# Performance work log

Measured on AMD Instinct MI355X. Metric: run time of the kernel, lower is better.

The kernel has to match this reference:

```python
import jax, jax.numpy as jnp
import numpy as np

NUM_ITER = 3
HEADS = 8
EPS = 1e-8

def _ln(x, g, b, eps=1e-5):
    mu = x.mean(-1, keepdims=True)
    var = ((x - mu) ** 2).mean(-1, keepdims=True)
    return (x - mu) * jax.lax.rsqrt(var + eps) * g + b

def setup_inputs() -> dict:
    key = jax.random.key(0)
    ks = jax.random.split(key, 10)
    B, Nkv, Din = 32, 4096, 256
    Nq, S, Hm = 16, 256, 512
    def xav(k, shape):
        lim = (6.0 / (shape[0] + shape[1])) ** 0.5
        return jax.random.uniform(k, shape, minval=-lim, maxval=lim, dtype=jnp.float32)
    return {
        "slots": jax.random.normal(ks[0], (Nq, S), dtype=jnp.float32),
        "inputs": jax.random.normal(ks[1], (B, Nkv, Din), dtype=jnp.float32),
        "norm_in_g": jnp.ones((Din,), jnp.float32), "norm_in_b": jnp.zeros((Din,), jnp.float32),
        "norm_slots_g": jnp.ones((S,), jnp.float32), "norm_slots_b": jnp.zeros((S,), jnp.float32),
        "norm_mlp_g": jnp.ones((S,), jnp.float32), "norm_mlp_b": jnp.zeros((S,), jnp.float32),
        "Wq": xav(ks[2], (S, S)), "Wk": xav(ks[3], (S, Din)), "Wv": xav(ks[4], (S, Din)),
        "gru_wih": xav(ks[5], (3 * S, S)),
        "gru_whh": jax.random.normal(ks[6], (3 * S, S), dtype=jnp.float32) * (1.0 / S ** 0.5),
        "gru_bih": jnp.zeros((3 * S,), jnp.float32), "gru_bhh": jnp.zeros((3 * S,), jnp.float32),
        "mlp_w1": xav(ks[7], (Hm, S)), "mlp_b1": jnp.zeros((Hm,), jnp.float32),
        "mlp_w2": xav(ks[8], (S, Hm)), "mlp_b2": jnp.zeros((S,), jnp.float32),
    }

def reference(slots, inputs, norm_in_g, norm_in_b, norm_slots_g, norm_slots_b,
              norm_mlp_g, norm_mlp_b, Wq, Wk, Wv, gru_wih, gru_whh, gru_bih, gru_bhh,
              mlp_w1, mlp_b1, mlp_w2, mlp_b2):
    B, Nkv, Din = inputs.shape
    Nq, S = slots.shape
    H = HEADS
    hd = S // H
    slots = jnp.broadcast_to(slots, (B, Nq, S))
    x = _ln(inputs, norm_in_g, norm_in_b)
    k = (x @ Wk.T).reshape(B, Nkv, H, hd).transpose(0, 2, 1, 3) * (hd ** -0.5)  # [B,H,Nkv,hd]
    v = (x @ Wv.T).reshape(B, Nkv, H, hd).transpose(0, 2, 1, 3)
    attn_vis = None
    for _ in range(NUM_ITER):
        slots_prev = slots
        s = _ln(slots, norm_slots_g, norm_slots_b)
        q = (s @ Wq.T).reshape(B, Nq, H, hd).transpose(0, 2, 1, 3)  # [B,H,Nq,hd]
        # logits [B,Nkv,H*Nq]; softmax jointly over heads and slots per key (slot-axis softmax)
        logits = jnp.einsum('bhkd,bhqd->bkhq', k, q).reshape(B, Nkv, H * Nq)
        attn = jax.nn.softmax(logits, axis=-1).reshape(B, Nkv, H, Nq).transpose(0, 2, 1, 3)  # [B,H,Nkv,Nq]
        attn_vis = attn.sum(1)  # [B,Nkv,Nq]
        attn_n = attn / (attn.sum(axis=2, keepdims=True) + EPS)  # normalize over keys
        updates = jnp.einsum('bhkq,bhkd->bqhd', attn_n, v).reshape(B, Nq, S)
        # GRUCell: gates order r,z,n
        xg = updates.reshape(-1, S)
        h = slots_prev.reshape(-1, S)
        gi = xg @ gru_wih.T + gru_bih
        gh = h @ gru_whh.T + gru_bhh
        ir, iz, inn = jnp.split(gi, 3, axis=-1)
        hr, hz, hn = jnp.split(gh, 3, axis=-1)
        r = jax.nn.sigmoid(ir + hr)
        z = jax.nn.sigmoid(iz + hz)
        n = jnp.tanh(inn + r * hn)
        slots = ((1.0 - z) * n + z * h).reshape(B, Nq, S)
        m = _ln(slots, norm_mlp_g, norm_mlp_b)
        slots = slots + (jax.nn.relu(m @ mlp_w1.T + mlp_b1) @ mlp_w2.T + mlp_b2)
    return (slots, attn_vis)
```

## Files before the change

### kernel.cpp

```cpp
#include <hip/hip_runtime.h>
#include <stdint.h>

typedef unsigned short u16;
typedef __attribute__((ext_vector_type(8))) _Float16 half8;
typedef __attribute__((ext_vector_type(4))) _Float16 half4;
typedef __attribute__((ext_vector_type(4))) float floatx4;

__device__ inline float bflo(unsigned u){ return __uint_as_float(u << 16); }
__device__ inline float bfhi(unsigned u){ return __uint_as_float(u & 0xffff0000u); }
__device__ inline float bf1(u16 v){ return __uint_as_float(((unsigned)v) << 16); }
__device__ inline u16 f2bf(float f){
  unsigned u = __float_as_uint(f);
  u += 0x7fffu + ((u >> 16) & 1u);
  return (u16)(u >> 16);
}
__device__ inline float dot8(uint4 w, float4 a, float4 b, float acc){
  acc = fmaf(bflo(w.x), a.x, acc); acc = fmaf(bfhi(w.x), a.y, acc);
  acc = fmaf(bflo(w.y), a.z, acc); acc = fmaf(bfhi(w.y), a.w, acc);
  acc = fmaf(bflo(w.z), b.x, acc); acc = fmaf(bfhi(w.z), b.y, acc);
  acc = fmaf(bflo(w.w), b.z, acc); acc = fmaf(bfhi(w.w), b.w, acc);
  return acc;
}

#define CW_SLOTS 0
#define CW_GIN   4096
#define CW_BIN   4352
#define CW_GS    4608
#define CW_BS    4864
#define CW_GM    5120
#define CW_BM    5376
#define CW_WQ    5632
#define CW_WK    71168
#define CW_WV    136704
#define CW_WIH   202240
#define CW_WHH   398848
#define CW_BIH   595456
#define CW_BHH   596224
#define CW_W1    596992
#define CW_B1    728064
#define CW_W2    728576
#define CW_B2    859648
#define CW_TOTAL 859904

__global__ void k_flag(const u16* __restrict__ probe, int* __restrict__ flag){
  int t = threadIdx.x;
  int bad = 0;
  #pragma unroll
  for (int i = 0; i < 4; i++){
    float x = bf1(probe[t + i * 256]);
    if (!(fabsf(x) < 1e6f)) bad = 1;
  }
  __shared__ int s;
  if (t == 0) s = 0;
  __syncthreads();
  if (bad) atomicOr(&s, 1);
  __syncthreads();
  if (t == 0) *flag = s;
}

struct CanonArgs { const void* p[18]; };

__global__ void k_canon(CanonArgs a, const int* __restrict__ flag, u16* __restrict__ cw){
  const int off[19] = {CW_SLOTS, CW_GIN, CW_BIN, CW_GS, CW_BS, CW_GM, CW_BM, CW_WQ,
                       CW_WK, CW_WV, CW_WIH, CW_WHH, CW_BIH, CW_BHH, CW_W1, CW_B1,
                       CW_W2, CW_B2, CW_TOTAL};
  int i = blockIdx.x * 256 + threadIdx.x;
  if (i >= CW_TOTAL) return;
  int f32m = *flag;
  int j = 0;
  while (i >= off[j + 1]) j++;
  int local = i - off[j];
  float v = f32m ? ((const float*)a.p[j])[local] : bf1(((const u16*)a.p[j])[local]);
  cw[i] = f2bf(v);
}

__global__ void k_init(const u16* __restrict__ cw, float* __restrict__ slots,
                       _Float16* __restrict__ wkvh)
{
  int idx = blockIdx.x * 256 + threadIdx.x;
  if (idx < 131072){
    float g = bf1(cw[CW_GIN + (idx & 255)]);
    wkvh[idx] = (_Float16)(bf1(cw[CW_WK + idx]) * g);
  } else {
    int i = idx - 131072;
    int d = i & 255;
    int q = (i >> 8) & 15;
    slots[i] = bf1(cw[CW_SLOTS + q * 256 + d]);
  }
}

__global__ void k_beta(const u16* __restrict__ cw, float* __restrict__ beta,
                       float* __restrict__ colsum){
  int c = blockIdx.x * 256 + threadIdx.x;
  if (c >= 512) return;
  float a = 0.f, s = 0.f;
  for (int d = 0; d < 256; d++){
    float w = bf1(cw[CW_WK + c * 256 + d]);
    a = fmaf(bf1(cw[CW_BIN + d]), w, a);
    s = fmaf(bf1(cw[CW_GIN + d]), w, s);
  }
  beta[c] = a;
  colsum[c] = s;
}

__global__ void k_zero(float* __restrict__ p, int n){
  int i = blockIdx.x * 256 + threadIdx.x;
  if (i < n) p[i] = 0.f;
}

template<int F32>
__device__ __forceinline__ void k1_body(
    const void* __restrict__ inp, const float* __restrict__ beta,
    const float* __restrict__ colsum, const _Float16* __restrict__ Bl,
    _Float16* __restrict__ kh, _Float16* __restrict__ vT,
    int nb, long rowb0, int colW, int wc, int m16, int q4, int lane)
{
  constexpr int NR = F32 ? 16 : 8;
  float bet[4], cs[4];
  #pragma unroll
  for (int nt = 0; nt < 4; nt++){
    bet[nt] = beta[colW + nt * 16 + m16];
    cs[nt]  = colsum[colW + nt * 16 + m16];
  }
  long vbase = ((long)(rowb0 >> 12)) * 64 * 256;

  uint4 ra[NR], rb_[NR];

  auto LOAD = [&](long rowb, uint4* r){
    long myRow = rowb + m16;
    if (F32){
      const uint4* rp = (const uint4*)((const float*)inp + myRow * 256 + q4 * 8);
      #pragma unroll
      for (int s = 0; s < 8; s++){ r[2*s] = rp[s*8]; r[2*s+1] = rp[s*8+1]; }
    } else {
      const uint4* rp = (const uint4*)((const u16*)inp + myRow * 256 + q4 * 8);
      #pragma unroll
      for (int s = 0; s < 8; s++) r[s] = rp[s*4];
    }
  };

  auto PROCESS = [&](long rowb, uint4* r){
    float sum = 0.f, sq = 0.f;
    half8 af[8];
    if (F32){
      #pragma unroll
      for (int s = 0; s < 8; s++){
        float x[8] = { __uint_as_float(r[2*s].x), __uint_as_float(r[2*s].y),
                       __uint_as_float(r[2*s].z), __uint_as_float(r[2*s].w),
                       __uint_as_float(r[2*s+1].x), __uint_as_float(r[2*s+1].y),
                       __uint_as_float(r[2*s+1].z), __uint_as_float(r[2*s+1].w) };
        #pragma unroll
        for (int p = 0; p < 8; p++){
          sum += x[p]; sq = fmaf(x[p], x[p], sq);
          af[s][p] = (_Float16)x[p];
        }
      }
    } else {
      #pragma unroll
      for (int s = 0; s < 8; s++){
        unsigned xw[4] = {r[s].x, r[s].y, r[s].z, r[s].w};
        #pragma unroll
        for (int p = 0; p < 4; p++){
          float a = bflo(xw[p]), b = bfhi(xw[p]);
          sum += a + b; sq = fmaf(a, a, sq); sq = fmaf(b, b, sq);
          af[s][2*p]   = (_Float16)a;
          af[s][2*p+1] = (_Float16)b;
        }
      }
    }
    sum += __shfl_xor(sum, 16); sq += __shfl_xor(sq, 16);
    sum += __shfl_xor(sum, 32); sq += __shfl_xor(sq, 32);
    float mu = sum * (1.f/256.f);
    float rstd = rsqrtf(fmaf(-mu, mu, sq * (1.f/256.f)) + 1e-5f);

    floatx4 acc[4];
    #pragma unroll
    for (int nt = 0; nt < 4; nt++) acc[nt] = (floatx4)0.f;
    #pragma unroll
    for (int s = 0; s < 8; s++)
      #pragma unroll
      for (int nt = 0; nt < 4; nt++){
        half8 bfr = *(const half8*)(Bl + (((wc * 4 + nt) * 8 + s) * 64 + lane) * 8);
        acc[nt] = __builtin_amdgcn_mfma_f32_16x16x32_f16(af[s], bfr, acc[nt], 0, 0, 0);
      }

    float mur[4], rsr[4];
    #pragma unroll
    for (int r2 = 0; r2 < 4; r2++){
      mur[r2] = __shfl(mu,   q4 * 4 + r2);
      rsr[r2] = __shfl(rstd, q4 * 4 + r2);
    }
    #pragma unroll
    for (int nt = 0; nt < 4; nt++)
      #pragma unroll
      for (int r2 = 0; r2 < 4; r2++)
        acc[nt][r2] = fmaf(rsr[r2], fmaf(-mur[r2], cs[nt], acc[nt][r2]), bet[nt]);

    if (nb == 0){
      long crow = rowb + q4 * 4;
      #pragma unroll
      for (int nt = 0; nt < 4; nt++)
        #pragma unroll
        for (int r2 = 0; r2 < 4; r2++)
          kh[(crow + r2) * 256 + colW + nt * 16 + m16] = (_Float16)acc[nt][r2];
    } else {
      int kloc = (int)rowb & 4095;
      long kg = vbase + (long)(kloc >> 6) * 256;
      int klo = (kloc & 63) + q4 * 4;
      #pragma unroll
      for (int nt = 0; nt < 4; nt++){
        int cv = (colW - 256) + nt * 16 + m16;
        half4 pk;
        pk[0] = (_Float16)acc[nt][0]; pk[1] = (_Float16)acc[nt][1];
        pk[2] = (_Float16)acc[nt][2]; pk[3] = (_Float16)acc[nt][3];
        *(half4*)(vT + (kg + cv) * 64 + klo) = pk;
      }
    }
  };

  LOAD(rowb0, ra);
  #pragma unroll 1
  for (int rt = 0; rt < 16; rt += 2){
    LOAD(rowb0 + (rt + 1) * 16, rb_);
    PROCESS(rowb0 + rt * 16, ra);
    if (rt + 2 < 16) LOAD(rowb0 + (rt + 2) * 16, ra);
    PROCESS(rowb0 + (rt + 1) * 16, rb_);
  }
}

__global__ __launch_bounds__(512, 2) void k1_gemm(
    const void* __restrict__ inp, const int* __restrict__ flag,
    const float* __restrict__ beta, const float* __restrict__ colsum,
    const _Float16* __restrict__ wkvh, _Float16* __restrict__ kh, _Float16* __restrict__ vT)
{
  int tid = threadIdx.x;
  int wv = tid >> 6, lane = tid & 63;
  int m16 = lane & 15, q4 = lane >> 4;
  int wc = wv & 3, wr = wv >> 2;
  int nb = blockIdx.y;
  long rowb0 = (long)blockIdx.x * 512 + wr * 256;
  int colW = nb * 256 + wc * 64;

  __shared__ _Float16 Bl[65536];

  {
    const _Float16* wb = wkvh + (long)nb * 65536;
    #pragma unroll
    for (int i = 0; i < 16; i++){
      int f = i * 512 + tid;
      int lf = f & 63;
      int s  = (f >> 6) & 7;
      int ntw = f >> 9;
      int col = (ntw >> 2) * 64 + (ntw & 3) * 16 + (lf & 15);
      int k8  = s * 32 + (lf >> 4) * 8;
      *(half8*)(Bl + f * 8) = *(const half8*)(wb + col * 256 + k8);
    }
  }
  __syncthreads();

  if (*flag) k1_body<1>(inp, beta, colsum, Bl, kh, vT, nb, rowb0, colW, wc, m16, q4, lane);
  else       k1_body<0>(inp, beta, colsum, Bl, kh, vT, nb, rowb0, colW, wc, m16, q4, lane);
}

__global__ __launch_bounds__(256) void k2_q(
    const float* __restrict__ slots, const u16* __restrict__ cw, _Float16* __restrict__ qh)
{
  const u16* gq = cw + CW_GS;
  const u16* bq = cw + CW_BS;
  const u16* Wq = cw + CW_WQ;
  int row = blockIdx.x, tid = threadIdx.x;
  int wv = tid >> 6, lane = tid & 63;
  float x = slots[row * 256 + tid];
  float s = x, s2 = x * x;
  #pragma unroll
  for (int m = 1; m < 64; m <<= 1){ s += __shfl_xor(s, m); s2 += __shfl_xor(s2, m); }
  __shared__ float red[8];
  if (lane == 0){ red[wv] = s; red[4 + wv] = s2; }
  __syncthreads();
  float tot  = red[0] + red[1] + red[2] + red[3];
  float tot2 = red[4] + red[5] + red[6] + red[7];
  float mu = tot * (1.f/256.f);
  float rstd = rsqrtf(tot2 * (1.f/256.f) - mu * mu + 1e-5f);
  __shared__ float sln[256];
  sln[tid] = (x - mu) * rstd * bf1(gq[tid]) + bf1(bq[tid]);
  __syncthreads();
  const u16* wr = Wq + tid * 256;
  float a = 0.f;
  for (int k = 0; k < 256; k += 8){
    uint4 wu = *(const uint4*)(wr + k);
    float4 l0 = *(const float4*)(sln + k);
    float4 l1 = *(const float4*)(sln + k + 4);
    a = dot8(wu, l0, l1, a);
  }
  qh[row * 256 + tid] = (_Float16)(a * 0.17677669529663687f);
}

__global__ __launch_bounds__(256) void k3_attn(
    const _Float16* __restrict__ kh, const _Float16* __restrict__ vT,
    const _Float16* __restrict__ qh,
    float* __restrict__ denom, float* __restrict__ numer,
    void* __restrict__ out_base, const int* __restrict__ flag, int lastIter)
{
  int f32m = *flag;
  int tid = threadIdx.x;
  int wv = tid >> 6, lane = tid & 63;
  int m16 = lane & 15, q4 = lane >> 4;
  int b = blockIdx.y, chunk = blockIdx.x;
  __shared__ float lds_l[32 * 129];

  half8 qf[2];
  #pragma unroll
  for (int hh = 0; hh < 2; hh++){
    int h = wv * 2 + hh;
    qf[hh] = *(const half8*)(qh + (b * 16 + m16) * 256 + h * 32 + q4 * 8);
  }
  float pd[2] = {0.f, 0.f};
  floatx4 un[2][2];
  #pragma unroll
  for (int hh = 0; hh < 2; hh++)
    #pragma unroll
    for (int dt = 0; dt < 2; dt++) un[hh][dt] = (floatx4)0.f;

  floatx4 z4 = (floatx4)0.f;
  for (int g4 = 0; g4 < 8; g4++){
    int key0 = chunk * 256 + g4 * 32;
    #pragma unroll
    for (int sub = 0; sub < 2; sub++){
      long rowb = (long)b * 4096 + key0 + sub * 16;
      #pragma unroll
      for (int hh = 0; hh < 2; hh++){
        int h = wv * 2 + hh;
        half8 af = *(const half8*)(kh + (rowb + m16) * 256 + h * 32 + q4 * 8);
        floatx4 d = __builtin_amdgcn_mfma_f32_16x16x32_f16(af, qf[hh], z4, 0, 0, 0);
        #pragma unroll
        for (int r = 0; r < 4; r++)
          lds_l[(sub * 16 + q4 * 4 + r) * 129 + h * 16 + m16] = d[r];
      }
    }
    __syncthreads();
    {
      int qq = tid & 15;
      #pragma unroll
      for (int half_ = 0; half_ < 2; half_++){
        int kk = (tid >> 4) + half_ * 16;
        float l[8];
        #pragma unroll
        for (int h8 = 0; h8 < 8; h8++) l[h8] = lds_l[kk * 129 + h8 * 16 + qq];
        float M = l[0];
        #pragma unroll
        for (int h8 = 1; h8 < 8; h8++) M = fmaxf(M, l[h8]);
        #pragma unroll
        for (int msk = 1; msk < 16; msk <<= 1) M = fmaxf(M, __shfl_xor(M, msk));
        float p[8], sl = 0.f;
        #pragma unroll
        for (int h8 = 0; h8 < 8; h8++){ p[h8] = __expf(l[h8] - M); sl += p[h8]; }
        float St = sl;
        #pragma unroll
        for (int msk = 1; msk < 16; msk <<= 1) St += __shfl_xor(St, msk);
        float rS = 1.f / St;
        if (lastIter){
          float av = sl * rS;
          long idx = 131072 + ((long)b * 4096 + key0 + kk) * 16 + qq;
          if (f32m) ((float*)out_base)[idx] = av;
          else      ((u16*)out_base)[idx]   = f2bf(av);
        }
        #pragma unroll
        for (int h8 = 0; h8 < 8; h8++) lds_l[kk * 129 + h8 * 16 + qq] = p[h8] * rS;
      }
    }
    __syncthreads();
    int kg0 = key0 >> 6;
    int kr  = (key0 & 63) + q4 * 8;
    #pragma unroll
    for (int hh = 0; hh < 2; hh++){
      int h = wv * 2 + hh;
      float pv[8];
      #pragma unroll
      for (int j = 0; j < 8; j++) pv[j] = lds_l[(q4 * 8 + j) * 129 + h * 16 + m16];
      float ps = 0.f;
      #pragma unroll
      for (int j = 0; j < 8; j++) ps += pv[j];
      pd[hh] += ps;
      half8 bfr;
      #pragma unroll
      for (int j = 0; j < 8; j++) bfr[j] = (_Float16)pv[j];
      #pragma unroll
      for (int dt = 0; dt < 2; dt++){
        half8 afr = *(const half8*)(vT + (((long)b * 64 + kg0) * 256 + h * 32 + dt * 16 + m16) * 64 + kr);
        un[hh][dt] = __builtin_amdgcn_mfma_f32_16x16x32_f16(afr, bfr, un[hh][dt], 0, 0, 0);
      }
    }
    __syncthreads();
  }
  #pragma unroll
  for (int hh = 0; hh < 2; hh++){
    int h = wv * 2 + hh;
    float t = pd[hh];
    t += __shfl_xor(t, 16); t += __shfl_xor(t, 32);
    if (q4 == 0) atomicAdd(&denom[(b * 8 + h) * 16 + m16], t);
    #pragma unroll
    for (int dt = 0; dt < 2; dt++)
      #pragma unroll
      for (int r = 0; r < 4; r++)
        atomicAdd(&numer[((b * 8 + h) * 16 + m16) * 32 + dt * 16 + q4 * 4 + r], un[hh][dt][r]);
  }
}

__global__ __launch_bounds__(256) void k4a_gru(
    const float* __restrict__ slots, const float* __restrict__ numer, const float* __restrict__ denom,
    const u16* __restrict__ cw, float* __restrict__ mid)
{
  const u16* wih = cw + CW_WIH;
  const u16* whh = cw + CW_WHH;
  const u16* bih = cw + CW_BIH;
  const u16* bhh = cw + CW_BHH;
  int jc = blockIdx.x, rg = blockIdx.y;
  int tid = threadIdx.x;
  __shared__ float u_s[8][256];
  __shared__ float h_s[8][256];
  {
    int hh = tid >> 5, dh = tid & 31;
    for (int i = 0; i < 8; i++){
      int row = rg * 8 + i;
      int b = row >> 4, slot = row & 15;
      float den = denom[(b * 8 + hh) * 16 + slot] + 1e-8f;
      u_s[i][tid] = numer[((b * 8 + hh) * 16 + slot) * 32 + dh] / den;
      h_s[i][tid] = slots[row * 256 + tid];
    }
  }
  __syncthreads();
  int rl = tid >> 5, jl = tid & 31;
  int j = jc * 32 + jl;
  int row = rg * 8 + rl;
  const u16* wir = wih + j * 256;
  const u16* wiz = wih + (256 + j) * 256;
  const u16* win = wih + (512 + j) * 256;
  const u16* whr = whh + j * 256;
  const u16* whz = whh + (256 + j) * 256;
  const u16* whn = whh + (512 + j) * 256;
  float air = 0, aiz = 0, ain = 0, ahr = 0, ahz = 0, ahn = 0;
  for (int k = 0; k < 256; k += 8){
    float4 u0 = *(const float4*)(&u_s[rl][k]);
    float4 u1 = *(const float4*)(&u_s[rl][k + 4]);
    float4 h0 = *(const float4*)(&h_s[rl][k]);
    float4 h1 = *(const float4*)(&h_s[rl][k + 4]);
    air = dot8(*(const uint4*)(wir + k), u0, u1, air);
    aiz = dot8(*(const uint4*)(wiz + k), u0, u1, aiz);
    ain = dot8(*(const uint4*)(win + k), u0, u1, ain);
    ahr = dot8(*(const uint4*)(whr + k), h0, h1, ahr);
    ahz = dot8(*(const uint4*)(whz + k), h0, h1, ahz);
    ahn = dot8(*(const uint4*)(whn + k), h0, h1, ahn);
  }
  float gr = air + bf1(bih[j])       + ahr + bf1(bhh[j]);
  float gz = aiz + bf1(bih[256 + j]) + ahz + bf1(bhh[256 + j]);
  float r = 1.f / (1.f + __expf(-gr));
  float z = 1.f / (1.f + __expf(-gz));
  float nn = tanhf(ain + bf1(bih[512 + j]) + r * (ahn + bf1(bhh[512 + j])));
  float h = h_s[rl][j];
  mid[row * 256 + j] = (1.f - z) * nn + z * h;
}

__global__ __launch_bounds__(256) void k4b_mlp(
    const float* __restrict__ mid, const u16* __restrict__ cw,
    float* __restrict__ slots, void* __restrict__ out_base,
    const int* __restrict__ flag, int lastIter)
{
  int f32m = *flag;
  const u16* gm = cw + CW_GM;
  const u16* bm = cw + CW_BM;
  const u16* w1 = cw + CW_W1;
  const u16* b1 = cw + CW_B1;
  const u16* w2 = cw + CW_W2;
  const u16* b2 = cw + CW_B2;
  int row = blockIdx.x, tid = threadIdx.x;
  int wv = tid >> 6, lane = tid & 63;
  float x = mid[row * 256 + tid];
  float s = x, s2 = x * x;
  #pragma unroll
  for (int m = 1; m < 64; m <<= 1){ s += __shfl_xor(s, m); s2 += __shfl_xor(s2, m); }
  __shared__ float red[8];
  if (lane == 0){ red[wv] = s; red[4 + wv] = s2; }
  __syncthreads();
  float tot  = red[0] + red[1] + red[2] + red[3];
  float tot2 = red[4] + red[5] + red[6] + red[7];
  float mu = tot * (1.f/256.f);
  float rstd = rsqrtf(tot2 * (1.f/256.f) - mu * mu + 1e-5f);
  __shared__ float ls[256];
  __shared__ float h1[512];
  ls[tid] = (x - mu) * rstd * bf1(gm[tid]) + bf1(bm[tid]);
  __syncthreads();
  const u16* w1a = w1 + tid * 256;
  const u16* w1b = w1 + (tid + 256) * 256;
  float a0 = 0.f, a1 = 0.f;
  for (int k = 0; k < 256; k += 8){
    float4 l0 = *(const float4*)(ls + k);
    float4 l1 = *(const float4*)(ls + k + 4);
    a0 = dot8(*(const uint4*)(w1a + k), l0, l1, a0);
    a1 = dot8(*(const uint4*)(w1b + k), l0, l1, a1);
  }
  h1[tid]       = fmaxf(a0 + bf1(b1[tid]), 0.f);
  h1[tid + 256] = fmaxf(a1 + bf1(b1[tid + 256]), 0.f);
  __syncthreads();
  const u16* w2r = w2 + tid * 512;
  float a = 0.f;
  for (int k = 0; k < 512; k += 8){
    float4 l0 = *(const float4*)(h1 + k);
    float4 l1 = *(const float4*)(h1 + k + 4);
    a = dot8(*(const uint4*)(w2r + k), l0, l1, a);
  }
  float res = x + a + bf1(b2[tid]);
  slots[row * 256 + tid] = res;
  if (lastIter){
    int idx = row * 256 + tid;
    if (f32m) ((float*)out_base)[idx] = res;
    else      ((u16*)out_base)[idx]   = f2bf(res);
  }
}

extern "C" void kernel_launch(void* const* d_in, const int* in_sizes, int n_in,
                              void* d_out, int out_size, void* d_ws, size_t ws_size,
                              hipStream_t stream)
{
  char* ws = (char*)d_ws;
  int*  flagp    = (int*)ws;
  u16*  cw       = (u16*)(ws + 256);
  _Float16* qh   = (_Float16*)(ws + 1720064);
  _Float16* wkvh = (_Float16*)(ws + 1982208);
  float* slots   = (float*)(ws + 2244352);
  float* mid     = (float*)(ws + 2768640);
  float* numer   = (float*)(ws + 3292928);
  float* denom   = (float*)(ws + 3817216);
  _Float16* kh   = (_Float16*)(ws + 3833600);
  _Float16* vT   = (_Float16*)(ws + 70942464);
  float*  beta   = (float*)(ws + 3817216);
  float*  colsum = beta + 512;

  CanonArgs ca;
  ca.p[0]  = d_in[0];   ca.p[1]  = d_in[2];   ca.p[2]  = d_in[3];
  ca.p[3]  = d_in[4];   ca.p[4]  = d_in[5];   ca.p[5]  = d_in[6];
  ca.p[6]  = d_in[7];   ca.p[7]  = d_in[8];   ca.p[8]  = d_in[9];
  ca.p[9]  = d_in[10];  ca.p[10] = d_in[11];  ca.p[11] = d_in[12];
  ca.p[12] = d_in[13];  ca.p[13] = d_in[14];  ca.p[14] = d_in[15];
  ca.p[15] = d_in[16];  ca.p[16] = d_in[17];  ca.p[17] = d_in[18];

  k_flag<<<1, 256, 0, stream>>>((const u16*)d_in[1], flagp);
  k_canon<<<(CW_TOTAL + 255) / 256, 256, 0, stream>>>(ca, flagp, cw);
  k_init<<<1024, 256, 0, stream>>>(cw, slots, wkvh);
  k_beta<<<2, 256, 0, stream>>>(cw, beta, colsum);
  k1_gemm<<<dim3(256, 2), 512, 0, stream>>>(d_in[1], flagp, beta, colsum, wkvh, kh, vT);
  for (int it = 0; it < 3; it++){
    int last = (it == 2) ? 1 : 0;
    k2_q<<<512, 256, 0, stream>>>(slots, cw, qh);
    k_zero<<<528, 256, 0, stream>>>(numer, 135168);
    k3_attn<<<dim3(16, 32), 256, 0, stream>>>(kh, vT, qh, denom, numer, d_out, flagp, last);
    k4a_gru<<<dim3(8, 64), 256, 0, stream>>>(slots, numer, denom, cw, mid);
    k4b_mlp<<<512, 256, 0, stream>>>(mid, cw, slots, d_out, flagp, last);
  }
}
```

Before: 907.7 us.

## Restructure K/V projection GEMM to register-held weights with smaller blocks

The K/V projection kernel no longer stages a 128KB weight tile in LDS. Each wave now holds its 16-column weight fragment in registers and processes 128 rows over a much larger grid (1024x8 blocks of 256 threads). The vT layout becomes a plain [B,256,4096] transpose, and the attention kernel's grid axes are swapped, presumably so consecutive blocks share a batch. The input rows are now re-read by 8 column blocks instead of 2, which increases global/L2 traffic in exchange for occupancy and no LDS staging.

After: 1.146 ms. 26.3% more time.

```diff
diff --git a/kernel.cpp b/kernel.cpp
--- a/kernel.cpp
+++ b/kernel.cpp
@@ -111,44 +111,44 @@
 template<int F32>
 __device__ __forceinline__ void k1_body(
     const void* __restrict__ inp, const float* __restrict__ beta,
-    const float* __restrict__ colsum, const _Float16* __restrict__ Bl,
+    const float* __restrict__ colsum, const _Float16* __restrict__ wkvh,
     _Float16* __restrict__ kh, _Float16* __restrict__ vT,
-    int nb, long rowb0, int colW, int wc, int m16, int q4, int lane)
-{
+    int nb, long rowb0, int colW, int m16, int q4)
+{
+  half8 bfr[8];
+  #pragma unroll
+  for (int s = 0; s < 8; s++)
+    bfr[s] = *(const half8*)(wkvh + (colW + m16) * 256 + s * 32 + q4 * 8);
+  float bet = beta[colW + m16];
+  float cs  = colsum[colW + m16];
+
   constexpr int NR = F32 ? 16 : 8;
-  float bet[4], cs[4];
-  #pragma unroll
-  for (int nt = 0; nt < 4; nt++){
-    bet[nt] = beta[colW + nt * 16 + m16];
-    cs[nt]  = colsum[colW + nt * 16 + m16];
-  }
-  long vbase = ((long)(rowb0 >> 12)) * 64 * 256;
-
-  uint4 ra[NR], rb_[NR];
-
-  auto LOAD = [&](long rowb, uint4* r){
+  uint4 raw[NR];
+  half8 af[8];
+  float sum = 0.f, sq = 0.f;
+
+  auto ISSUE = [&](long rowb){
     long myRow = rowb + m16;
     if (F32){
       const uint4* rp = (const uint4*)((const float*)inp + myRow * 256 + q4 * 8);
       #pragma unroll
-      for (int s = 0; s < 8; s++){ r[2*s] = rp[s*8]; r[2*s+1] = rp[s*8+1]; }
+      for (int s = 0; s < 8; s++){ raw[2*s] = rp[s*8]; raw[2*s+1] = rp[s*8+1]; }
     } else {
       const uint4* rp = (const uint4*)((const u16*)inp + myRow * 256 + q4 * 8);
       #pragma unroll
-      for (int s = 0; s < 8; s++) r[s] = rp[s*4];
+      for (int s = 0; s < 8; s++) raw[s] = rp[s*4];
     }
   };
 
-  auto PROCESS = [&](long rowb, uint4* r){
-    float sum = 0.f, sq = 0.f;
-    half8 af[8];
+  auto CONVERT = [&](){
+    sum = 0.f; sq = 0.f;
     if (F32){
       #pragma unroll
       for (int s = 0; s < 8; s++){
-        float x[8] = { __uint_as_float(r[2*s].x), __uint_as_float(r[2*s].y),
-                       __uint_as_float(r[2*s].z), __uint_as_float(r[2*s].w),
-                       __uint_as_float(r[2*s+1].x), __uint_as_float(r[2*s+1].y),
-                       __uint_as_float(r[2*s+1].z), __uint_as_float(r[2*s+1].w) };
+        float x[8] = { __uint_as_float(raw[2*s].x), __uint_as_float(raw[2*s].y),
+                       __uint_as_float(raw[2*s].z), __uint_as_float(raw[2*s].w),
+                       __uint_as_float(raw[2*s+1].x), __uint_as_float(raw[2*s+1].y),
+                       __uint_as_float(raw[2*s+1].z), __uint_as_float(raw[2*s+1].w) };
         #pragma unroll
         for (int p = 0; p < 8; p++){
           sum += x[p]; sq = fmaf(x[p], x[p], sq);
@@ -158,7 +158,7 @@
     } else {
       #pragma unroll
       for (int s = 0; s < 8; s++){
-        unsigned xw[4] = {r[s].x, r[s].y, r[s].z, r[s].w};
+        unsigned xw[4] = {raw[s].x, raw[s].y, raw[s].z, raw[s].w};
         #pragma unroll
         for (int p = 0; p < 4; p++){
           float a = bflo(xw[p]), b = bfhi(xw[p]);
@@ -168,21 +168,19 @@
         }
       }
     }
-    sum += __shfl_xor(sum, 16); sq += __shfl_xor(sq, 16);
-    sum += __shfl_xor(sum, 32); sq += __shfl_xor(sq, 32);
-    float mu = sum * (1.f/256.f);
-    float rstd = rsqrtf(fmaf(-mu, mu, sq * (1.f/256.f)) + 1e-5f);
-
-    floatx4 acc[4];
-    #pragma unroll
-    for (int nt = 0; nt < 4; nt++) acc[nt] = (floatx4)0.f;
+  };
+
+  auto COMPUTE = [&](long rowb){
+    float s1 = sum, s2 = sq;
+    s1 += __shfl_xor(s1, 16); s2 += __shfl_xor(s2, 16);
+    s1 += __shfl_xor(s1, 32); s2 += __shfl_xor(s2, 32);
+    float mu = s1 * (1.f/256.f);
+    float rstd = rsqrtf(fmaf(-mu, mu, s2 * (1.f/256.f)) + 1e-5f);
+
+    floatx4 acc = (floatx4)0.f;
     #pragma unroll
     for (int s = 0; s < 8; s++)
-      #pragma unroll
-      for (int nt = 0; nt < 4; nt++){
-        half8 bfr = *(const half8*)(Bl + (((wc * 4 + nt) * 8 + s) * 64 + lane) * 8);
-        acc[nt] = __builtin_amdgcn_mfma_f32_16x16x32_f16(af[s], bfr, acc[nt], 0, 0, 0);
-      }
+      acc = __builtin_amdgcn_mfma_f32_16x16x32_f16(af[s], bfr[s], acc, 0, 0, 0);
 
     float mur[4], rsr[4];
     #pragma unroll
@@ -191,44 +189,36 @@
       rsr[r2] = __shfl(rstd, q4 * 4 + r2);
     }
     #pragma unroll
-    for (int nt = 0; nt < 4; nt++)
+    for (int r2 = 0; r2 < 4; r2++)
+      acc[r2] = fmaf(rsr[r2], fmaf(-mur[r2], cs, acc[r2]), bet);
+
+    if (nb < 4){
+      long crow = rowb + q4 * 4;
       #pragma unroll
       for (int r2 = 0; r2 < 4; r2++)
-        acc[nt][r2] = fmaf(rsr[r2], fmaf(-mur[r2], cs[nt], acc[nt][r2]), bet[nt]);
-
-    if (nb == 0){
-      long crow = rowb + q4 * 4;
-      #pragma unroll
-      for (int nt = 0; nt < 4; nt++)
-        #pragma unroll
-        for (int r2 = 0; r2 < 4; r2++)
-          kh[(crow + r2) * 256 + colW + nt * 16 + m16] = (_Float16)acc[nt][r2];
+        kh[(crow + r2) * 256 + colW + m16] = (_Float16)acc[r2];
     } else {
-      int kloc = (int)rowb & 4095;
-      long kg = vbase + (long)(kloc >> 6) * 256;
-      int klo = (kloc & 63) + q4 * 4;
-      #pragma unroll
-      for (int nt = 0; nt < 4; nt++){
-        int cv = (colW - 256) + nt * 16 + m16;
-        half4 pk;
-        pk[0] = (_Float16)acc[nt][0]; pk[1] = (_Float16)acc[nt][1];
-        pk[2] = (_Float16)acc[nt][2]; pk[3] = (_Float16)acc[nt][3];
-        *(half4*)(vT + (kg + cv) * 64 + klo) = pk;
-      }
+      int b = (int)(rowb >> 12);
+      int key = ((int)rowb & 4095) + q4 * 4;
+      int cv = (colW - 256) + m16;
+      half4 pk;
+      pk[0] = (_Float16)acc[0]; pk[1] = (_Float16)acc[1];
+      pk[2] = (_Float16)acc[2]; pk[3] = (_Float16)acc[3];
+      *(half4*)(vT + ((long)b * 256 + cv) * 4096 + key) = pk;
     }
   };
 
-  LOAD(rowb0, ra);
+  ISSUE(rowb0);
+  CONVERT();
   #pragma unroll 1
-  for (int rt = 0; rt < 16; rt += 2){
-    LOAD(rowb0 + (rt + 1) * 16, rb_);
-    PROCESS(rowb0 + rt * 16, ra);
-    if (rt + 2 < 16) LOAD(rowb0 + (rt + 2) * 16, ra);
-    PROCESS(rowb0 + (rt + 1) * 16, rb_);
-  }
-}
-
-__global__ __launch_bounds__(512, 2) void k1_gemm(
+  for (int rt = 0; rt < 8; rt++){
+    if (rt < 7) ISSUE(rowb0 + (rt + 1) * 16);
+    COMPUTE(rowb0 + rt * 16);
+    if (rt < 7) CONVERT();
+  }
+}
+
+__global__ __launch_bounds__(256) void k1_gemm(
     const void* __restrict__ inp, const int* __restrict__ flag,
     const float* __restrict__ beta, const float* __restrict__ colsum,
     const _Float16* __restrict__ wkvh, _Float16* __restrict__ kh, _Float16* __restrict__ vT)
@@ -236,30 +226,12 @@
   int tid = threadIdx.x;
   int wv = tid >> 6, lane = tid & 63;
   int m16 = lane & 15, q4 = lane >> 4;
-  int wc = wv & 3, wr = wv >> 2;
   int nb = blockIdx.y;
-  long rowb0 = (long)blockIdx.x * 512 + wr * 256;
-  int colW = nb * 256 + wc * 64;
-
-  __shared__ _Float16 Bl[65536];
-
-  {
-    const _Float16* wb = wkvh + (long)nb * 65536;
-    #pragma unroll
-    for (int i = 0; i < 16; i++){
-      int f = i * 512 + tid;
-      int lf = f & 63;
-      int s  = (f >> 6) & 7;
-      int ntw = f >> 9;
-      int col = (ntw >> 2) * 64 + (ntw & 3) * 16 + (lf & 15);
-      int k8  = s * 32 + (lf >> 4) * 8;
-      *(half8*)(Bl + f * 8) = *(const half8*)(wb + col * 256 + k8);
-    }
-  }
-  __syncthreads();
-
-  if (*flag) k1_body<1>(inp, beta, colsum, Bl, kh, vT, nb, rowb0, colW, wc, m16, q4, lane);
-  else       k1_body<0>(inp, beta, colsum, Bl, kh, vT, nb, rowb0, colW, wc, m16, q4, lane);
+  long rowb0 = (long)blockIdx.x * 128;
+  int colW = nb * 64 + wv * 16;
+
+  if (*flag) k1_body<1>(inp, beta, colsum, wkvh, kh, vT, nb, rowb0, colW, m16, q4);
+  else       k1_body<0>(inp, beta, colsum, wkvh, kh, vT, nb, rowb0, colW, m16, q4);
 }
 
 __global__ __launch_bounds__(256) void k2_q(
@@ -305,7 +277,7 @@
   int tid = threadIdx.x;
   int wv = tid >> 6, lane = tid & 63;
   int m16 = lane & 15, q4 = lane >> 4;
-  int b = blockIdx.y, chunk = blockIdx.x;
+  int b = blockIdx.x, chunk = blockIdx.y;
   __shared__ float lds_l[32 * 129];
 
   half8 qf[2];
@@ -369,8 +341,6 @@
       }
     }
     __syncthreads();
-    int kg0 = key0 >> 6;
-    int kr  = (key0 & 63) + q4 * 8;
     #pragma unroll
     for (int hh = 0; hh < 2; hh++){
       int h = wv * 2 + hh;
@@ -386,7 +356,7 @@
       for (int j = 0; j < 8; j++) bfr[j] = (_Float16)pv[j];
       #pragma unroll
       for (int dt = 0; dt < 2; dt++){
-        half8 afr = *(const half8*)(vT + (((long)b * 64 + kg0) * 256 + h * 32 + dt * 16 + m16) * 64 + kr);
+        half8 afr = *(const half8*)(vT + ((long)b * 256 + h * 32 + dt * 16 + m16) * 4096 + key0 + q4 * 8);
         un[hh][dt] = __builtin_amdgcn_mfma_f32_16x16x32_f16(afr, bfr, un[hh][dt], 0, 0, 0);
       }
     }
@@ -547,12 +517,12 @@
   k_canon<<<(CW_TOTAL + 255) / 256, 256, 0, stream>>>(ca, flagp, cw);
   k_init<<<1024, 256, 0, stream>>>(cw, slots, wkvh);
   k_beta<<<2, 256, 0, stream>>>(cw, beta, colsum);
-  k1_gemm<<<dim3(256, 2), 512, 0, stream>>>(d_in[1], flagp, beta, colsum, wkvh, kh, vT);
+  k1_gemm<<<dim3(1024, 8), 256, 0, stream>>>(d_in[1], flagp, beta, colsum, wkvh, kh, vT);
   for (int it = 0; it < 3; it++){
     int last = (it == 2) ? 1 : 0;
     k2_q<<<512, 256, 0, stream>>>(slots, cw, qh);
     k_zero<<<528, 256, 0, stream>>>(numer, 135168);
-    k3_attn<<<dim3(16, 32), 256, 0, stream>>>(kh, vT, qh, denom, numer, d_out, flagp, last);
+    k3_attn<<<dim3(32, 16), 256, 0, stream>>>(kh, vT, qh, denom, numer, d_out, flagp, last);
     k4a_gru<<<dim3(8, 64), 256, 0, stream>>>(slots, numer, denom, cw, mid);
     k4b_mlp<<<512, 256, 0, stream>>>(mid, cw, slots, d_out, flagp, last);
   }
```
